# Performance work log

Hardware: AMD Instinct MI355X
Metric: run time of the kernel (lower is better)

Reference implementation:

```python
import jax, jax.numpy as jnp
import numpy as np


def setup_inputs() -> dict:
    key = jax.random.key(0)
    k1, k2, k3, k4, k5 = jax.random.split(key, 5)
    B, S, I, O, R = 4, 2048, 4096, 4096, 16
    s = 1.0 / np.sqrt(I)
    return {
        "x": jax.random.normal(k1, (B, S, I), dtype=jnp.float32),
        "W": jax.random.normal(k2, (O, I), dtype=jnp.float32) * s,
        "b": jax.random.normal(k3, (O,), dtype=jnp.float32) * 0.02,
        "lora_A": jax.random.normal(k4, (I, R), dtype=jnp.float32) * s,
        "lora_B": jax.random.normal(k5, (R, O), dtype=jnp.float32) * 0.02,
    }


def reference(x, W, b, lora_A, lora_B):
    # Base linear: F.linear(x, W, b) = x @ W.T + b   -> [B, S, O]
    base_out = jnp.einsum("bsi,oi->bso", x, W) + b
    # LoRA low-rank delta: (x @ A) @ B  -> [B, S, O]
    lora_out = jnp.einsum("bsr,ro->bso", jnp.einsum("bsi,ir->bsr", x, lora_A), lora_B)
    return base_out + lora_out
```

## Files before the change

### kernel.cpp

```cpp
#include <hip/hip_runtime.h>

typedef float f32x4 __attribute__((ext_vector_type(4)));
typedef __bf16 bf16x8 __attribute__((ext_vector_type(8)));
typedef __bf16 bf16x4 __attribute__((ext_vector_type(4)));

#define GLOBAL_AS __attribute__((address_space(1)))
#define LDS_AS    __attribute__((address_space(3)))

static __device__ __forceinline__ void gload16(const void* g, void* l) {
  __builtin_amdgcn_global_load_lds((const GLOBAL_AS void*)g, (LDS_AS void*)l, 16, 0, 0);
}

#define BAR() __builtin_amdgcn_s_barrier()
#define WAITL0() do { asm volatile("s_waitcnt lgkmcnt(0)" ::: "memory"); __builtin_amdgcn_sched_barrier(0); } while (0)
#define WAITL8() do { asm volatile("s_waitcnt lgkmcnt(8)" ::: "memory"); __builtin_amdgcn_sched_barrier(0); } while (0)

__global__ __launch_bounds__(256)
void prep_all(const float* __restrict__ X, const float* __restrict__ A,
              const float* __restrict__ W, const float* __restrict__ Bl,
              __bf16* __restrict__ Xb, __bf16* __restrict__ XAb,
              __bf16* __restrict__ Wb, __bf16* __restrict__ BlT) {
  __shared__ float Xs[16][68];
  __shared__ float At[16][68];
  const int bid = blockIdx.x;
  const int t = threadIdx.x;
  if (bid < 512) {
    constexpr int K = 4096, KC = 64;
    const int m0 = bid * 16;
    const int lrow = t >> 4, c4 = (t & 15) * 4;
    const int orow = t >> 4, oc = t & 15;
    const int akk = t >> 2, ar4 = (t & 3) * 4;
    f32x4 av = (f32x4)0.f;
    for (int k0 = 0; k0 < K; k0 += KC) {
      f32x4 u = *reinterpret_cast<const f32x4*>(X + (size_t)(m0 + lrow) * K + k0 + c4);
      *reinterpret_cast<f32x4*>(&Xs[lrow][c4]) = u;
      bf16x4 p;
#pragma unroll
      for (int e = 0; e < 4; ++e) p[e] = (__bf16)u[e];
      *reinterpret_cast<bf16x4*>(Xb + (size_t)(m0 + lrow) * K + k0 + c4) = p;
      f32x4 a = *reinterpret_cast<const f32x4*>(A + (size_t)(k0 + akk) * 16 + ar4);
      At[ar4 + 0][akk] = a[0]; At[ar4 + 1][akk] = a[1];
      At[ar4 + 2][akk] = a[2]; At[ar4 + 3][akk] = a[3];
      __syncthreads();
#pragma unroll
      for (int q = 0; q < 16; ++q) {
        f32x4 xv = *reinterpret_cast<const f32x4*>(&Xs[orow][q * 4]);
        av += xv * *reinterpret_cast<const f32x4*>(&At[oc][q * 4]);
      }
      __syncthreads();
    }
    const float acc = av[0] + av[1] + av[2] + av[3];
    const size_t base = (size_t)(m0 + orow) * 64;
    XAb[base + oc] = (__bf16)acc;
#pragma unroll
    for (int z = 0; z < 3; ++z) XAb[base + 16 + z * 16 + oc] = (__bf16)0.f;
  } else if (bid < 1536) {
    long base = (long)(bid - 512) * 256 + t;
#pragma unroll
    for (int r = 0; r < 8; ++r) {
      long i = base + (long)r * 262144;
      f32x4 u = reinterpret_cast<const f32x4*>(W)[2 * i];
      f32x4 v = reinterpret_cast<const f32x4*>(W)[2 * i + 1];
      bf16x8 p;
#pragma unroll
      for (int e = 0; e < 4; ++e) { p[e] = (__bf16)u[e]; p[4 + e] = (__bf16)v[e]; }
      reinterpret_cast<bf16x8*>(Wb)[i] = p;
    }
  } else {
    int idx = (bid - 1536) * 256 + t;
    int col = idx >> 6, k = idx & 63;
    float v = (k < 16) ? Bl[(size_t)k * 4096 + col] : 0.f;
    BlT[idx] = (__bf16)v;
  }
}

__global__ __launch_bounds__(512, 2)
void gemm8(const __bf16* __restrict__ Xb, const __bf16* __restrict__ Wb,
           const __bf16* __restrict__ XAb, const __bf16* __restrict__ BlT,
           const float* __restrict__ bias, float* __restrict__ out) {
  constexpr int N = 4096;
  __shared__ __align__(16) char sm[131072];
  char* Asm_ = sm;
  char* Bsm_ = sm + 65536;

  const int t = threadIdx.x;
  const int lane = t & 63, w = t >> 6;
  const int wr = w >> 2, wc = w & 3;
  const int fr = lane & 15, fg = lane >> 4;

  const int bid = blockIdx.x;
  const int xcd = bid & 7, l = bid >> 3;
  const int mt = (xcd << 2) | ((l >> 4) & 2) | (l & 1);
  const int nt = (l >> 1) & 15;
  const int m0 = mt * 256, n0 = nt * 256;

  const int sRow = w * 16 + (lane >> 2);
  const int sColB = (((lane & 3) ^ ((lane >> 3) & 3)) << 4);
  const int rdOff = fr * 64 + ((fg ^ ((fr >> 1) & 3)) << 4);
  const int rdOffA = wr * 16384 + rdOff;
  const int rdOffB = (wc >> 1) * 16384 + (wc & 1) * 8192 + rdOff;

  const char* gA0 = (const char*)Xb + (size_t)(m0 + sRow) * 8192 + sColB;
  const char* gA1 = (const char*)Xb + (size_t)(m0 + 128 + sRow) * 8192 + sColB;
  const char* gB0 = (const char*)Wb + (size_t)(n0 + sRow) * 8192 + sColB;
  const char* gB1 = (const char*)Wb + (size_t)(n0 + 128 + sRow) * 8192 + sColB;

  auto stage2 = [&](const char* g, char* dst) { gload16(g, dst); gload16(g + 64, dst + 1024); };

  auto rdA = [&](int b, int mf, int kk) -> bf16x8 {
    return *reinterpret_cast<const bf16x8*>(Asm_ + b * 32768 + (mf * 2 + kk) * 1024 + rdOffA);
  };
  auto rdB = [&](int b, int nf, int kk) -> bf16x8 {
    return *reinterpret_cast<const bf16x8*>(Bsm_ + b * 32768 + (nf * 2 + kk) * 1024 + rdOffB);
  };

  f32x4 acc[8][4];
#pragma unroll
  for (int i = 0; i < 8; ++i)
#pragma unroll
    for (int j = 0; j < 4; ++j) acc[i][j] = (f32x4)0.f;

  bf16x8 aLo[4][2], aHi[4][2], bLo[2][2], bHi[2][2];

  auto MF = [&](bf16x8 (&af)[4][2], bf16x8 (&bf_)[2][2], int mi, int ni) {
#pragma unroll
    for (int i = 0; i < 4; ++i)
#pragma unroll
      for (int j = 0; j < 2; ++j)
#pragma unroll
        for (int kk = 0; kk < 2; ++kk)
          acc[mi * 4 + i][ni * 2 + j] = __builtin_amdgcn_mfma_f32_16x16x32_bf16(
              af[i][kk], bf_[j][kk], acc[mi * 4 + i][ni * 2 + j], 0, 0, 0);
  };

  float bb[4];
#pragma unroll
  for (int j = 0; j < 4; ++j) bb[j] = bias[n0 + wc * 64 + j * 16 + fr];

  stage2(gA0, Asm_ + w * 2048);
  stage2(gA1, Asm_ + 16384 + w * 2048);
  stage2(gB0, Bsm_ + w * 2048);
  stage2(gB1, Bsm_ + 16384 + w * 2048);
  stage2(gB0 + 128, Bsm_ + 32768 + w * 2048);
  stage2(gB1 + 128, Bsm_ + 32768 + 16384 + w * 2048);
  asm volatile("s_waitcnt vmcnt(4)" ::: "memory");
  BAR();

  const char* pA0 = gA0 + 128;
  const char* pA1 = gA1 + 128;
  const char* pB0 = gB0 + 256;
  const char* pB1 = gB1 + 256;

  auto tile_step = [&](int b) {
    char* dstA = Asm_ + (b ^ 1) * 32768 + w * 2048;
    char* dstB = Bsm_ + b * 32768 + w * 2048;
#pragma unroll
    for (int i = 0; i < 4; ++i)
#pragma unroll
      for (int kk = 0; kk < 2; ++kk) aLo[i][kk] = rdA(b, i, kk);
#pragma unroll
    for (int j = 0; j < 2; ++j)
#pragma unroll
      for (int kk = 0; kk < 2; ++kk) bLo[j][kk] = rdB(b, j, kk);
    stage2(pA0, dstA); pA0 += 128;
    asm volatile("s_waitcnt lgkmcnt(8)" ::: "memory");
    BAR(); WAITL0();
    __builtin_amdgcn_s_setprio(1); MF(aLo, bLo, 0, 0); __builtin_amdgcn_s_setprio(0);
#pragma unroll
    for (int j = 0; j < 2; ++j)
#pragma unroll
      for (int kk = 0; kk < 2; ++kk) bHi[j][kk] = rdB(b, 2 + j, kk);
#pragma unroll
    for (int i = 0; i < 4; ++i)
#pragma unroll
      for (int kk = 0; kk < 2; ++kk) aHi[i][kk] = rdA(b, 4 + i, kk);
    BAR();
    stage2(pA1, dstA + 16384); pA1 += 128;
    WAITL8();
    __builtin_amdgcn_s_setprio(1); MF(aLo, bHi, 0, 1); __builtin_amdgcn_s_setprio(0);
    BAR();
    stage2(pB0, dstB); pB0 += 128;
    WAITL0();
    __builtin_amdgcn_s_setprio(1); MF(aHi, bHi, 1, 1); __builtin_amdgcn_s_setprio(0);
    BAR();
    stage2(pB1, dstB + 16384); pB1 += 128;
    __builtin_amdgcn_s_setprio(1); MF(aHi, bLo, 1, 0); __builtin_amdgcn_s_setprio(0);
    asm volatile("s_waitcnt vmcnt(4)" ::: "memory");
    BAR();
  };

  for (int tp = 0; tp < 31; ++tp) { tile_step(0); tile_step(1); }

  {
    const char* gBl0 = (const char*)BlT + (size_t)(n0 + sRow) * 128 + sColB;
    const char* gBl1 = (const char*)BlT + (size_t)(n0 + 128 + sRow) * 128 + sColB;
    char* dstA = Asm_ + 32768 + w * 2048;
    char* dstB = Bsm_ + w * 2048;
#pragma unroll
    for (int i = 0; i < 4; ++i)
#pragma unroll
      for (int kk = 0; kk < 2; ++kk) aLo[i][kk] = rdA(0, i, kk);
#pragma unroll
    for (int j = 0; j < 2; ++j)
#pragma unroll
      for (int kk = 0; kk < 2; ++kk) bLo[j][kk] = rdB(0, j, kk);
    stage2(pA0, dstA);
    BAR(); WAITL0();
    __builtin_amdgcn_s_setprio(1); MF(aLo, bLo, 0, 0); __builtin_amdgcn_s_setprio(0);
    BAR();
#pragma unroll
    for (int j = 0; j < 2; ++j)
#pragma unroll
      for (int kk = 0; kk < 2; ++kk) bHi[j][kk] = rdB(0, 2 + j, kk);
    stage2(pA1, dstA + 16384);
    BAR(); WAITL0();
    __builtin_amdgcn_s_setprio(1); MF(aLo, bHi, 0, 1); __builtin_amdgcn_s_setprio(0);
    BAR();
#pragma unroll
    for (int i = 0; i < 4; ++i)
#pragma unroll
      for (int kk = 0; kk < 2; ++kk) aHi[i][kk] = rdA(0, 4 + i, kk);
    stage2(gBl0, dstB);
    BAR(); WAITL0();
    __builtin_amdgcn_s_setprio(1); MF(aHi, bHi, 1, 1); __builtin_amdgcn_s_setprio(0);
    BAR();
    stage2(gBl1, dstB + 16384);
    BAR(); WAITL0();
    __builtin_amdgcn_s_setprio(1); MF(aHi, bLo, 1, 0); __builtin_amdgcn_s_setprio(0);
    asm volatile("s_waitcnt vmcnt(4)" ::: "memory");
    BAR();
  }

  {
    const char* gXA0 = (const char*)XAb + (size_t)(m0 + sRow) * 128 + sColB;
    const char* gXA1 = (const char*)XAb + (size_t)(m0 + 128 + sRow) * 128 + sColB;
    char* dstA = Asm_ + w * 2048;
#pragma unroll
    for (int i = 0; i < 4; ++i)
#pragma unroll
      for (int kk = 0; kk < 2; ++kk) aLo[i][kk] = rdA(1, i, kk);
#pragma unroll
    for (int j = 0; j < 2; ++j)
#pragma unroll
      for (int kk = 0; kk < 2; ++kk) bLo[j][kk] = rdB(1, j, kk);
    stage2(gXA0, dstA);
    BAR(); WAITL0();
    __builtin_amdgcn_s_setprio(1); MF(aLo, bLo, 0, 0); __builtin_amdgcn_s_setprio(0);
    BAR();
#pragma unroll
    for (int j = 0; j < 2; ++j)
#pragma unroll
      for (int kk = 0; kk < 2; ++kk) bHi[j][kk] = rdB(1, 2 + j, kk);
    stage2(gXA1, dstA + 16384);
    BAR(); WAITL0();
    __builtin_amdgcn_s_setprio(1); MF(aLo, bHi, 0, 1); __builtin_amdgcn_s_setprio(0);
    BAR();
#pragma unroll
    for (int i = 0; i < 4; ++i)
#pragma unroll
      for (int kk = 0; kk < 2; ++kk) aHi[i][kk] = rdA(1, 4 + i, kk);
    BAR(); WAITL0();
    __builtin_amdgcn_s_setprio(1); MF(aHi, bHi, 1, 1); __builtin_amdgcn_s_setprio(0);
    BAR();
    __builtin_amdgcn_s_setprio(1); MF(aHi, bLo, 1, 0); __builtin_amdgcn_s_setprio(0);
    BAR();
  }

  asm volatile("s_waitcnt vmcnt(0)" ::: "memory");
  BAR();
  {
#pragma unroll
    for (int i = 0; i < 4; ++i)
#pragma unroll
      for (int kk = 0; kk < 2; ++kk) aLo[i][kk] = rdA(0, i, kk);
#pragma unroll
    for (int j = 0; j < 2; ++j)
#pragma unroll
      for (int kk = 0; kk < 2; ++kk) { bLo[j][kk] = rdB(0, j, kk); bHi[j][kk] = rdB(0, 2 + j, kk); }
    MF(aLo, bLo, 0, 0); MF(aLo, bHi, 0, 1);
#pragma unroll
    for (int i = 0; i < 4; ++i)
#pragma unroll
      for (int kk = 0; kk < 2; ++kk) aHi[i][kk] = rdA(0, 4 + i, kk);
    MF(aHi, bHi, 1, 1); MF(aHi, bLo, 1, 0);
  }

#pragma unroll
  for (int i = 0; i < 8; ++i) {
    const int row0 = m0 + wr * 128 + i * 16 + fg * 4;
#pragma unroll
    for (int j = 0; j < 4; ++j) {
      const int col = n0 + wc * 64 + j * 16 + fr;
#pragma unroll
      for (int q = 0; q < 4; ++q)
        out[(size_t)(row0 + q) * N + col] = acc[i][j][q] + bb[j];
    }
  }
}

extern "C" void kernel_launch(void* const* d_in, const int* in_sizes, int n_in,
                              void* d_out, int out_size, void* d_ws, size_t ws_size,
                              hipStream_t stream) {
  const float* x  = (const float*)d_in[0];
  const float* W  = (const float*)d_in[1];
  const float* b  = (const float*)d_in[2];
  const float* lA = (const float*)d_in[3];
  const float* lB = (const float*)d_in[4];
  float* out = (float*)d_out;

  char* ws = (char*)d_ws;
  __bf16* Xb  = (__bf16*)ws;
  __bf16* Wb  = (__bf16*)(ws + 67108864);
  __bf16* XAb = (__bf16*)(ws + 100663296);
  __bf16* BlT = (__bf16*)(ws + 101711872);

  prep_all<<<2560, 256, 0, stream>>>(x, lA, W, lB, Xb, XAb, Wb, BlT);
  gemm8<<<dim3(512), dim3(512), 0, stream>>>(Xb, Wb, XAb, BlT, b, out);
}
```

Measured before the change: 317.0 us.

## Restructure GEMM main loop into k-split halves with fewer barriers

Each tile step now issues all LDS fragment reads at once (all 8 A and 4 B fragments for both k-halves), then runs the k0 MFMA block after a partial lgkmcnt wait and the k1 block after the full wait. This replaces four quadrant MFMA phases and about four barriers per step with two phases and two barriers, meant to cut synchronization overhead and let LDS reads overlap with MFMAs. In exchange all fragments are held in registers at once, which raises VGPR pressure, and the global-to-LDS staging is reordered relative to the barriers, which carries a risk of write-after-read hazards on the LDS buffers.

```diff
diff --git a/kernel.cpp b/kernel.cpp
--- a/kernel.cpp
+++ b/kernel.cpp
@@ -12,8 +12,7 @@
 }
 
 #define BAR() __builtin_amdgcn_s_barrier()
-#define WAITL0() do { asm volatile("s_waitcnt lgkmcnt(0)" ::: "memory"); __builtin_amdgcn_sched_barrier(0); } while (0)
-#define WAITL8() do { asm volatile("s_waitcnt lgkmcnt(8)" ::: "memory"); __builtin_amdgcn_sched_barrier(0); } while (0)
+#define WAITL(n) do { asm volatile("s_waitcnt lgkmcnt(" #n ")" ::: "memory"); __builtin_amdgcn_sched_barrier(0); } while (0)
 
 __global__ __launch_bounds__(256)
 void prep_all(const float* __restrict__ X, const float* __restrict__ A,
@@ -120,17 +119,31 @@
 #pragma unroll
     for (int j = 0; j < 4; ++j) acc[i][j] = (f32x4)0.f;
 
-  bf16x8 aLo[4][2], aHi[4][2], bLo[2][2], bHi[2][2];
-
-  auto MF = [&](bf16x8 (&af)[4][2], bf16x8 (&bf_)[2][2], int mi, int ni) {
-#pragma unroll
-    for (int i = 0; i < 4; ++i)
-#pragma unroll
-      for (int j = 0; j < 2; ++j)
-#pragma unroll
-        for (int kk = 0; kk < 2; ++kk)
-          acc[mi * 4 + i][ni * 2 + j] = __builtin_amdgcn_mfma_f32_16x16x32_bf16(
-              af[i][kk], bf_[j][kk], acc[mi * 4 + i][ni * 2 + j], 0, 0, 0);
+  bf16x8 aK0[8], aK1[8], bK0[4], bK1[4];
+
+  auto MFk0 = [&]() {
+#pragma unroll
+    for (int mf = 0; mf < 8; ++mf)
+#pragma unroll
+      for (int nf = 0; nf < 4; ++nf)
+        acc[mf][nf] = __builtin_amdgcn_mfma_f32_16x16x32_bf16(aK0[mf], bK0[nf], acc[mf][nf], 0, 0, 0);
+  };
+  auto MFk1 = [&]() {
+#pragma unroll
+    for (int mf = 0; mf < 8; ++mf)
+#pragma unroll
+      for (int nf = 0; nf < 4; ++nf)
+        acc[mf][nf] = __builtin_amdgcn_mfma_f32_16x16x32_bf16(aK1[mf], bK1[nf], acc[mf][nf], 0, 0, 0);
+  };
+  auto RD = [&](int b) {
+#pragma unroll
+    for (int mf = 0; mf < 8; ++mf) aK0[mf] = rdA(b, mf, 0);
+#pragma unroll
+    for (int nf = 0; nf < 4; ++nf) bK0[nf] = rdB(b, nf, 0);
+#pragma unroll
+    for (int mf = 0; mf < 8; ++mf) aK1[mf] = rdA(b, mf, 1);
+#pragma unroll
+    for (int nf = 0; nf < 4; ++nf) bK1[nf] = rdB(b, nf, 1);
   };
 
   float bb[4];
@@ -154,37 +167,16 @@
   auto tile_step = [&](int b) {
     char* dstA = Asm_ + (b ^ 1) * 32768 + w * 2048;
     char* dstB = Bsm_ + b * 32768 + w * 2048;
-#pragma unroll
-    for (int i = 0; i < 4; ++i)
-#pragma unroll
-      for (int kk = 0; kk < 2; ++kk) aLo[i][kk] = rdA(b, i, kk);
-#pragma unroll
-    for (int j = 0; j < 2; ++j)
-#pragma unroll
-      for (int kk = 0; kk < 2; ++kk) bLo[j][kk] = rdB(b, j, kk);
+    RD(b);
     stage2(pA0, dstA); pA0 += 128;
-    asm volatile("s_waitcnt lgkmcnt(8)" ::: "memory");
-    BAR(); WAITL0();
-    __builtin_amdgcn_s_setprio(1); MF(aLo, bLo, 0, 0); __builtin_amdgcn_s_setprio(0);
-#pragma unroll
-    for (int j = 0; j < 2; ++j)
-#pragma unroll
-      for (int kk = 0; kk < 2; ++kk) bHi[j][kk] = rdB(b, 2 + j, kk);
-#pragma unroll
-    for (int i = 0; i < 4; ++i)
-#pragma unroll
-      for (int kk = 0; kk < 2; ++kk) aHi[i][kk] = rdA(b, 4 + i, kk);
-    BAR();
     stage2(pA1, dstA + 16384); pA1 += 128;
-    WAITL8();
-    __builtin_amdgcn_s_setprio(1); MF(aLo, bHi, 0, 1); __builtin_amdgcn_s_setprio(0);
+    WAITL(12);
+    __builtin_amdgcn_s_setprio(1); MFk0(); __builtin_amdgcn_s_setprio(0);
+    WAITL(0);
     BAR();
     stage2(pB0, dstB); pB0 += 128;
-    WAITL0();
-    __builtin_amdgcn_s_setprio(1); MF(aHi, bHi, 1, 1); __builtin_amdgcn_s_setprio(0);
-    BAR();
     stage2(pB1, dstB + 16384); pB1 += 128;
-    __builtin_amdgcn_s_setprio(1); MF(aHi, bLo, 1, 0); __builtin_amdgcn_s_setprio(0);
+    __builtin_amdgcn_s_setprio(1); MFk1(); __builtin_amdgcn_s_setprio(0);
     asm volatile("s_waitcnt vmcnt(4)" ::: "memory");
     BAR();
   };
@@ -192,97 +184,45 @@
   for (int tp = 0; tp < 31; ++tp) { tile_step(0); tile_step(1); }
 
   {
+    char* dstA = Asm_ + 32768 + w * 2048;
+    char* dstB = Bsm_ + w * 2048;
     const char* gBl0 = (const char*)BlT + (size_t)(n0 + sRow) * 128 + sColB;
     const char* gBl1 = (const char*)BlT + (size_t)(n0 + 128 + sRow) * 128 + sColB;
-    char* dstA = Asm_ + 32768 + w * 2048;
-    char* dstB = Bsm_ + w * 2048;
-#pragma unroll
-    for (int i = 0; i < 4; ++i)
-#pragma unroll
-      for (int kk = 0; kk < 2; ++kk) aLo[i][kk] = rdA(0, i, kk);
-#pragma unroll
-    for (int j = 0; j < 2; ++j)
-#pragma unroll
-      for (int kk = 0; kk < 2; ++kk) bLo[j][kk] = rdB(0, j, kk);
+    RD(0);
     stage2(pA0, dstA);
-    BAR(); WAITL0();
-    __builtin_amdgcn_s_setprio(1); MF(aLo, bLo, 0, 0); __builtin_amdgcn_s_setprio(0);
-    BAR();
-#pragma unroll
-    for (int j = 0; j < 2; ++j)
-#pragma unroll
-      for (int kk = 0; kk < 2; ++kk) bHi[j][kk] = rdB(0, 2 + j, kk);
     stage2(pA1, dstA + 16384);
-    BAR(); WAITL0();
-    __builtin_amdgcn_s_setprio(1); MF(aLo, bHi, 0, 1); __builtin_amdgcn_s_setprio(0);
-    BAR();
-#pragma unroll
-    for (int i = 0; i < 4; ++i)
-#pragma unroll
-      for (int kk = 0; kk < 2; ++kk) aHi[i][kk] = rdA(0, 4 + i, kk);
+    WAITL(12);
+    __builtin_amdgcn_s_setprio(1); MFk0(); __builtin_amdgcn_s_setprio(0);
+    WAITL(0);
+    BAR();
     stage2(gBl0, dstB);
-    BAR(); WAITL0();
-    __builtin_amdgcn_s_setprio(1); MF(aHi, bHi, 1, 1); __builtin_amdgcn_s_setprio(0);
-    BAR();
     stage2(gBl1, dstB + 16384);
-    BAR(); WAITL0();
-    __builtin_amdgcn_s_setprio(1); MF(aHi, bLo, 1, 0); __builtin_amdgcn_s_setprio(0);
+    __builtin_amdgcn_s_setprio(1); MFk1(); __builtin_amdgcn_s_setprio(0);
     asm volatile("s_waitcnt vmcnt(4)" ::: "memory");
     BAR();
   }
 
   {
+    char* dstA = Asm_ + w * 2048;
     const char* gXA0 = (const char*)XAb + (size_t)(m0 + sRow) * 128 + sColB;
     const char* gXA1 = (const char*)XAb + (size_t)(m0 + 128 + sRow) * 128 + sColB;
-    char* dstA = Asm_ + w * 2048;
-#pragma unroll
-    for (int i = 0; i < 4; ++i)
-#pragma unroll
-      for (int kk = 0; kk < 2; ++kk) aLo[i][kk] = rdA(1, i, kk);
-#pragma unroll
-    for (int j = 0; j < 2; ++j)
-#pragma unroll
-      for (int kk = 0; kk < 2; ++kk) bLo[j][kk] = rdB(1, j, kk);
+    RD(1);
     stage2(gXA0, dstA);
-    BAR(); WAITL0();
-    __builtin_amdgcn_s_setprio(1); MF(aLo, bLo, 0, 0); __builtin_amdgcn_s_setprio(0);
-    BAR();
-#pragma unroll
-    for (int j = 0; j < 2; ++j)
-#pragma unroll
-      for (int kk = 0; kk < 2; ++kk) bHi[j][kk] = rdB(1, 2 + j, kk);
     stage2(gXA1, dstA + 16384);
-    BAR(); WAITL0();
-    __builtin_amdgcn_s_setprio(1); MF(aLo, bHi, 0, 1); __builtin_amdgcn_s_setprio(0);
-    BAR();
-#pragma unroll
-    for (int i = 0; i < 4; ++i)
-#pragma unroll
-      for (int kk = 0; kk < 2; ++kk) aHi[i][kk] = rdA(1, 4 + i, kk);
-    BAR(); WAITL0();
-    __builtin_amdgcn_s_setprio(1); MF(aHi, bHi, 1, 1); __builtin_amdgcn_s_setprio(0);
-    BAR();
-    __builtin_amdgcn_s_setprio(1); MF(aHi, bLo, 1, 0); __builtin_amdgcn_s_setprio(0);
-    BAR();
-  }
-
-  asm volatile("s_waitcnt vmcnt(0)" ::: "memory");
-  BAR();
+    WAITL(12);
+    __builtin_amdgcn_s_setprio(1); MFk0(); __builtin_amdgcn_s_setprio(0);
+    WAITL(0);
+    __builtin_amdgcn_s_setprio(1); MFk1(); __builtin_amdgcn_s_setprio(0);
+    asm volatile("s_waitcnt vmcnt(0)" ::: "memory");
+    BAR();
+  }
+
   {
-#pragma unroll
-    for (int i = 0; i < 4; ++i)
-#pragma unroll
-      for (int kk = 0; kk < 2; ++kk) aLo[i][kk] = rdA(0, i, kk);
-#pragma unroll
-    for (int j = 0; j < 2; ++j)
-#pragma unroll
-      for (int kk = 0; kk < 2; ++kk) { bLo[j][kk] = rdB(0, j, kk); bHi[j][kk] = rdB(0, 2 + j, kk); }
-    MF(aLo, bLo, 0, 0); MF(aLo, bHi, 0, 1);
-#pragma unroll
-    for (int i = 0; i < 4; ++i)
-#pragma unroll
-      for (int kk = 0; kk < 2; ++kk) aHi[i][kk] = rdA(0, 4 + i, kk);
-    MF(aHi, bHi, 1, 1); MF(aHi, bLo, 1, 0);
+    RD(0);
+    WAITL(12);
+    MFk0();
+    WAITL(0);
+    MFk1();
   }
 
 #pragma unroll
```

New measurement: 321.5 us. Within noise of the previous version (+1.4%).
